# Kernel tuning notes

Hardware: AMD Instinct MI355X
Metric: run time of the kernel (lower is better)

Reference implementation:

```python
import jax, jax.numpy as jnp
import numpy as np

ALPHA = 0.25
GAMMA = 2.0
EPS = 1e-8
W_CLASS = 2.0
W_BBOX = 5.0
W_GIOU = 2.0
PROB_THRESH = 0.5
BBOX_THRESH = -0.1
BIG = 1e9  # cost assigned to filtered-out (masked) pseudo targets


def box_cxcywh_to_xyxy(b):
    cx, cy, w, h = b[..., 0], b[..., 1], b[..., 2], b[..., 3]
    return jnp.stack([cx - 0.5 * w, cy - 0.5 * h, cx + 0.5 * w, cy + 0.5 * h], axis=-1)


def generalized_box_iou(boxes1, boxes2):
    # boxes1: [..., N, 4] xyxy, boxes2: [..., M, 4] xyxy -> [..., N, M]
    area1 = (boxes1[..., 2] - boxes1[..., 0]) * (boxes1[..., 3] - boxes1[..., 1])
    area2 = (boxes2[..., 2] - boxes2[..., 0]) * (boxes2[..., 3] - boxes2[..., 1])
    lt = jnp.maximum(boxes1[..., :, None, :2], boxes2[..., None, :, :2])
    rb = jnp.minimum(boxes1[..., :, None, 2:], boxes2[..., None, :, 2:])
    wh = jnp.clip(rb - lt, 0.0)
    inter = wh[..., 0] * wh[..., 1]
    union = area1[..., :, None] + area2[..., None, :] - inter
    iou = inter / union
    lt_c = jnp.minimum(boxes1[..., :, None, :2], boxes2[..., None, :, :2])
    rb_c = jnp.maximum(boxes1[..., :, None, 2:], boxes2[..., None, :, 2:])
    wh_c = jnp.clip(rb_c - lt_c, 0.0)
    area_c = wh_c[..., 0] * wh_c[..., 1]
    return iou - (area_c - union) / area_c


def setup_inputs() -> dict:
    key = jax.random.key(0)
    k1, k2, k3, k4, k5 = jax.random.split(key, 5)
    B, Q, C, T = 32, 900, 91, 30
    return {
        "pred_logits": jax.random.normal(k1, (B, Q, C), dtype=jnp.float32),
        "pred_boxes": jax.random.uniform(k2, (B, Q, 4), dtype=jnp.float32),
        "pred_logits_base": jax.random.normal(k3, (B, Q, C), dtype=jnp.float32),
        "pred_boxes_base": jax.random.uniform(k4, (B, Q, 4), dtype=jnp.float32),
        "targets_boxes": jax.random.uniform(k5, (B, T, 4), dtype=jnp.float32),
    }


def reference(pred_logits, pred_boxes, pred_logits_base, pred_boxes_base, targets_boxes):
    # ---- pseudo-label generation from the base model (original: sort + python filter) ----
    prob_base = jax.nn.sigmoid(pred_logits_base)          # [B, Qb, C]
    top_prob = jnp.max(prob_base, axis=-1)                # [B, Qb]
    pseudo_labels = jnp.argmax(prob_base, axis=-1)        # [B, Qb] (idx_base[..., 0])
    keep_prob = top_prob > PROB_THRESH
    # original per-box loop: keep if all(-giou(pseudo, gt) > bbox_thresh)
    g_pt = generalized_box_iou(box_cxcywh_to_xyxy(pred_boxes_base),
                               box_cxcywh_to_xyxy(targets_boxes))  # [B, Qb, T]
    keep_giou = jnp.all(-g_pt > BBOX_THRESH, axis=-1)     # [B, Qb]
    pseudo_mask = keep_prob & keep_giou                   # valid pseudo-target slots

    # ---- cost matrix between current predictions and pseudo targets ----
    out_prob = jax.nn.sigmoid(pred_logits)                # [B, Q, C]
    # gather class prob at each pseudo target's label: [B, Q, Qb]
    p = jnp.take_along_axis(out_prob, pseudo_labels[:, None, :], axis=2)
    pos_cost = ALPHA * (1.0 - p) ** GAMMA * (-jnp.log(p + EPS))
    neg_cost = (1.0 - ALPHA) * p ** GAMMA * (-jnp.log(1.0 - p + EPS))
    cost_class = pos_cost - neg_cost

    # L1 cdist between cxcywh boxes: [B, Q, Qb]
    cost_bbox = jnp.sum(jnp.abs(pred_boxes[:, :, None, :] - pred_boxes_base[:, None, :, :]), axis=-1)

    cost_giou = -generalized_box_iou(box_cxcywh_to_xyxy(pred_boxes),
                                     box_cxcywh_to_xyxy(pred_boxes_base))  # [B, Q, Qb]

    C = W_BBOX * cost_bbox + W_CLASS * cost_class + W_GIOU * cost_giou
    # masked (filtered-out) pseudo targets get a huge cost so they are never matched
    C = jnp.where(pseudo_mask[:, None, :], C, BIG)
    return C, pseudo_mask
```

## Files before the change

### kernel.cpp

```cpp
#include <hip/hip_runtime.h>

typedef float f32x4 __attribute__((ext_vector_type(4)));

static constexpr int B  = 32;
static constexpr int Q  = 900;
static constexpr int NC = 91;
static constexpr int T  = 30;
static constexpr int QT = 12;

static constexpr float ALPHA_ = 0.25f;
static constexpr float EPS_   = 1e-8f;
static constexpr float BIG_   = 1e9f;

__global__ __launch_bounds__(256) void k1_mask_label(
    const float* __restrict__ logits_base,
    const float4* __restrict__ boxes_base,
    const float4* __restrict__ targets,
    int* __restrict__ labels,
    float* __restrict__ mask_out) {
#pragma clang fp contract(off)
  int wid  = (blockIdx.x * 256 + threadIdx.x) >> 6;
  int lane = threadIdx.x & 63;
  int b = wid / Q;

  const float* row = logits_base + (size_t)wid * NC;
  float v  = (lane < NC) ? row[lane] : -1e30f;
  int  arg = lane;
  int lane2 = lane + 64;
  if (lane2 < NC) {
    float v2 = row[lane2];
    if (v2 > v) { v = v2; arg = lane2; }
  }
  for (int off = 32; off >= 1; off >>= 1) {
    float ov = __shfl_xor(v, off, 64);
    int   oi = __shfl_xor(arg, off, 64);
    if (ov > v || (ov == v && oi < arg)) { v = ov; arg = oi; }
  }
  bool keep = (v > 0.0f);

  float4 bb = boxes_base[wid];
  float x1 = bb.x - 0.5f * bb.z, y1 = bb.y - 0.5f * bb.w;
  float x2 = bb.x + 0.5f * bb.z, y2 = bb.y + 0.5f * bb.w;
  float a1 = (x2 - x1) * (y2 - y1);

  bool ok = true;
  if (lane < T) {
    float4 tb = targets[b * T + lane];
    float tx1 = tb.x - 0.5f * tb.z, ty1 = tb.y - 0.5f * tb.w;
    float tx2 = tb.x + 0.5f * tb.z, ty2 = tb.y + 0.5f * tb.w;
    float a2 = (tx2 - tx1) * (ty2 - ty1);
    float ltx = fmaxf(x1, tx1), lty = fmaxf(y1, ty1);
    float rbx = fminf(x2, tx2), rby = fminf(y2, ty2);
    float iw = fmaxf(rbx - ltx, 0.0f), ih = fmaxf(rby - lty, 0.0f);
    float inter = iw * ih;
    float uni = (a1 + a2) - inter;
    float iou = inter / uni;
    float cx1 = fminf(x1, tx1), cy1 = fminf(y1, ty1);
    float cx2 = fmaxf(x2, tx2), cy2 = fmaxf(y2, ty2);
    float cw = fmaxf(cx2 - cx1, 0.0f), ch = fmaxf(cy2 - cy1, 0.0f);
    float ac = cw * ch;
    float g = iou - (ac - uni) / ac;
    ok = (-g > -0.1f);
  }
  keep = keep && __all(ok);

  if (lane == 0) {
    labels[wid]   = arg;
    mask_out[wid] = keep ? 1.0f : 0.0f;
  }
}

__device__ __forceinline__ float class_cost(float x) {
  float p   = __builtin_amdgcn_rcpf(1.0f + __expf(-x));
  float omp = 1.0f - p;
  float pos = ALPHA_ * (omp * omp) * (-__logf(p + EPS_));
  float neg = (1.0f - ALPHA_) * (p * p) * (-__logf(omp + EPS_));
  return pos - neg;
}

__global__ __launch_bounds__(256, 4) void k3_cost(
    const float* __restrict__ pred_logits,
    const float4* __restrict__ pred_boxes,
    const float4* __restrict__ boxes_base,
    const int* __restrict__ labels,
    const float* __restrict__ mask_in,
    float* __restrict__ Cout) {
  __shared__ float  s_cc[QT * NC];
  __shared__ float4 s_e[QT];
  __shared__ float4 s_m[QT];
  __shared__ float  s_pa[QT];

  int b   = blockIdx.x / (Q / QT);
  int q0  = (blockIdx.x % (Q / QT)) * QT;
  int tid = threadIdx.x;

  const f32x4* lg4 = reinterpret_cast<const f32x4*>(
      pred_logits + ((size_t)(b * Q + q0)) * NC);
  f32x4* sc4 = reinterpret_cast<f32x4*>(s_cc);
  for (int i = tid; i < QT * NC / 4; i += 256) {
    f32x4 v = __builtin_nontemporal_load(lg4 + i);
    f32x4 o;
    o.x = class_cost(v.x);
    o.y = class_cost(v.y);
    o.z = class_cost(v.z);
    o.w = class_cost(v.w);
    sc4[i] = o;
  }

  if (tid < QT) {
    float4 pb = pred_boxes[b * Q + q0 + tid];
    float px1 = pb.x - 0.5f * pb.z, py1 = pb.y - 0.5f * pb.w;
    float px2 = pb.x + 0.5f * pb.z, py2 = pb.y + 0.5f * pb.w;
    s_e[tid]  = make_float4(px1, py1, px2, py2);
    s_m[tid]  = make_float4(px1 + px2, py1 + py2, pb.z, pb.w);
    s_pa[tid] = (px2 - px1) * (py2 - py1);
  }

  bool active = (tid < Q / 4);
  float x1b[4], y1b[4], x2b[4], y2b[4], wb[4], hb[4], c2big[4];
  const float* pk[4];
  int jbase = b * Q + 4 * tid;
  if (active) {
    int4 lbv = *reinterpret_cast<const int4*>(labels + jbase);
    float4 mkv = *reinterpret_cast<const float4*>(mask_in + jbase);
    pk[0] = s_cc + lbv.x; pk[1] = s_cc + lbv.y;
    pk[2] = s_cc + lbv.z; pk[3] = s_cc + lbv.w;
    c2big[0] = 2.0f + (mkv.x != 0.0f ? 0.0f : BIG_);
    c2big[1] = 2.0f + (mkv.y != 0.0f ? 0.0f : BIG_);
    c2big[2] = 2.0f + (mkv.z != 0.0f ? 0.0f : BIG_);
    c2big[3] = 2.0f + (mkv.w != 0.0f ? 0.0f : BIG_);
#pragma unroll
    for (int k = 0; k < 4; ++k) {
      float4 bb = boxes_base[jbase + k];
      x1b[k] = bb.x - 0.5f * bb.z; y1b[k] = bb.y - 0.5f * bb.w;
      x2b[k] = bb.x + 0.5f * bb.z; y2b[k] = bb.y + 0.5f * bb.w;
      wb[k]  = bb.z; hb[k] = bb.w;
    }
  }
  __syncthreads();

  if (active) {
    size_t rowbase = ((size_t)(b * Q + q0)) * Q + 4 * tid;
#pragma unroll
    for (int qi = 0; qi < QT; ++qi, rowbase += Q) {
      float4 pe = s_e[qi];
      float4 pm = s_m[qi];
      float  pa = s_pa[qi];
      float res[4];
#pragma unroll
      for (int k = 0; k < 4; ++k) {
        float cls = pk[k][qi * NC];
        float dx = pm.x - (x1b[k] + x2b[k]);
        float dy = pm.y - (y1b[k] + y2b[k]);
        float dw = pm.z - wb[k];
        float dh = pm.w - hb[k];
        float l1 = fmaf(0.5f, fabsf(dx) + fabsf(dy), fabsf(dw) + fabsf(dh));
        float mwx = fminf(pe.z, x2b[k]) - fmaxf(pe.x, x1b[k]);
        float mwy = fminf(pe.w, y2b[k]) - fmaxf(pe.y, y1b[k]);
        float inter = fmaxf(mwx, 0.0f) * fmaxf(mwy, 0.0f);
        float uni = fmaf(wb[k], hb[k], pa) - inter;
        float cw = (pm.z + wb[k]) - mwx;
        float ch = (pm.w + hb[k]) - mwy;
        float acl = cw * ch;
        float r = __builtin_amdgcn_rcpf(uni * acl);
        float t = fmaf(inter, acl, uni * uni) * r;
        res[k] = fmaf(-2.0f, t, fmaf(5.0f, l1, fmaf(2.0f, cls, c2big[k])));
      }
      *reinterpret_cast<float4*>(Cout + rowbase) =
          make_float4(res[0], res[1], res[2], res[3]);
    }
  }
}

extern "C" void kernel_launch(void* const* d_in, const int* in_sizes, int n_in,
                              void* d_out, int out_size, void* d_ws, size_t ws_size,
                              hipStream_t stream) {
  const float*  pred_logits      = (const float*)d_in[0];
  const float4* pred_boxes       = (const float4*)d_in[1];
  const float*  pred_logits_base = (const float*)d_in[2];
  const float4* pred_boxes_base  = (const float4*)d_in[3];
  const float4* targets          = (const float4*)d_in[4];

  float* out      = (float*)d_out;
  float* mask_out = out + (size_t)B * Q * Q;

  int* labels = (int*)d_ws;

  k1_mask_label<<<(B * Q) / 4, 256, 0, stream>>>(
      pred_logits_base, pred_boxes_base, targets, labels, mask_out);

  k3_cost<<<B * (Q / QT), 256, 0, stream>>>(
      pred_logits, pred_boxes, pred_boxes_base, labels, mask_out, out);
}
```

Before: 48.24 us.

## Fuse mask/label and cost kernels into one cooperative persistent kernel with grid sync

Merges the pseudo-label/mask kernel and the cost-matrix kernel into a single persistent cooperative launch. Blocks first grid-stride over all pseudo-target rows, then a grid-wide barrier separates that phase from a grid-stride loop over cost tiles. This removes the second kernel launch and the gap between kernels, at the cost of a grid barrier, a fixed grid of up to 4 blocks per CU (assuming 256 CUs), and an extra __syncthreads per tile. The fallback path launches k3_cost twice, which is redundant but only runs if the cooperative launch fails.

```diff
diff --git a/kernel.cpp b/kernel.cpp
--- a/kernel.cpp
+++ b/kernel.cpp
@@ -1,4 +1,7 @@
 #include <hip/hip_runtime.h>
+#include <hip/hip_cooperative_groups.h>
+
+namespace cg = cooperative_groups;
 
 typedef float f32x4 __attribute__((ext_vector_type(4)));
 
@@ -12,15 +15,15 @@
 static constexpr float EPS_   = 1e-8f;
 static constexpr float BIG_   = 1e9f;
 
-__global__ __launch_bounds__(256) void k1_mask_label(
-    const float* __restrict__ logits_base,
-    const float4* __restrict__ boxes_base,
-    const float4* __restrict__ targets,
-    int* __restrict__ labels,
-    float* __restrict__ mask_out) {
+static constexpr int NTILES = B * (Q / QT);
+
+__device__ void mask_label_body(int wid, int lane,
+                                const float* __restrict__ logits_base,
+                                const float4* __restrict__ boxes_base,
+                                const float4* __restrict__ targets,
+                                int* __restrict__ labels,
+                                float* __restrict__ mask_out) {
 #pragma clang fp contract(off)
-  int wid  = (blockIdx.x * 256 + threadIdx.x) >> 6;
-  int lane = threadIdx.x & 63;
   int b = wid / Q;
 
   const float* row = logits_base + (size_t)wid * NC;
@@ -78,21 +81,17 @@
   return pos - neg;
 }
 
-__global__ __launch_bounds__(256, 4) void k3_cost(
-    const float* __restrict__ pred_logits,
-    const float4* __restrict__ pred_boxes,
-    const float4* __restrict__ boxes_base,
-    const int* __restrict__ labels,
-    const float* __restrict__ mask_in,
-    float* __restrict__ Cout) {
-  __shared__ float  s_cc[QT * NC];
-  __shared__ float4 s_e[QT];
-  __shared__ float4 s_m[QT];
-  __shared__ float  s_pa[QT];
-
-  int b   = blockIdx.x / (Q / QT);
-  int q0  = (blockIdx.x % (Q / QT)) * QT;
-  int tid = threadIdx.x;
+__device__ void cost_tile_body(int tile, int tid,
+                               const float* __restrict__ pred_logits,
+                               const float4* __restrict__ pred_boxes,
+                               const float4* __restrict__ boxes_base,
+                               const int* __restrict__ labels,
+                               const float* __restrict__ mask_in,
+                               float* __restrict__ Cout,
+                               float* s_cc, float4* s_e, float4* s_m,
+                               float* s_pa) {
+  int b  = tile / (Q / QT);
+  int q0 = (tile % (Q / QT)) * QT;
 
   const f32x4* lg4 = reinterpret_cast<const f32x4*>(
       pred_logits + ((size_t)(b * Q + q0)) * NC);
@@ -170,6 +169,64 @@
           make_float4(res[0], res[1], res[2], res[3]);
     }
   }
+  __syncthreads();
+}
+
+__global__ __launch_bounds__(256, 4) void fused_all(
+    const float* __restrict__ logits_base,
+    const float4* __restrict__ boxes_base,
+    const float4* __restrict__ targets,
+    int* __restrict__ labels,
+    float* __restrict__ mask_out,
+    const float* __restrict__ pred_logits,
+    const float4* __restrict__ pred_boxes,
+    float* __restrict__ Cout) {
+  __shared__ float  s_cc[QT * NC];
+  __shared__ float4 s_e[QT];
+  __shared__ float4 s_m[QT];
+  __shared__ float  s_pa[QT];
+
+  int tid  = threadIdx.x;
+  int lane = tid & 63;
+
+  int nwaves = gridDim.x * 4;
+  int gw = (blockIdx.x * 256 + tid) >> 6;
+  for (int wid = gw; wid < B * Q; wid += nwaves)
+    mask_label_body(wid, lane, logits_base, boxes_base, targets,
+                    labels, mask_out);
+
+  __threadfence();
+  cg::this_grid().sync();
+
+  for (int tile = blockIdx.x; tile < NTILES; tile += gridDim.x)
+    cost_tile_body(tile, tid, pred_logits, pred_boxes, boxes_base,
+                   labels, mask_out, Cout, s_cc, s_e, s_m, s_pa);
+}
+
+__global__ __launch_bounds__(256) void k1_mask_label(
+    const float* __restrict__ logits_base,
+    const float4* __restrict__ boxes_base,
+    const float4* __restrict__ targets,
+    int* __restrict__ labels,
+    float* __restrict__ mask_out) {
+  int wid  = (blockIdx.x * 256 + threadIdx.x) >> 6;
+  mask_label_body(wid, threadIdx.x & 63, logits_base, boxes_base, targets,
+                  labels, mask_out);
+}
+
+__global__ __launch_bounds__(256, 4) void k3_cost(
+    const float* __restrict__ pred_logits,
+    const float4* __restrict__ pred_boxes,
+    const float4* __restrict__ boxes_base,
+    const int* __restrict__ labels,
+    const float* __restrict__ mask_in,
+    float* __restrict__ Cout) {
+  __shared__ float  s_cc[QT * NC];
+  __shared__ float4 s_e[QT];
+  __shared__ float4 s_m[QT];
+  __shared__ float  s_pa[QT];
+  cost_tile_body(blockIdx.x, threadIdx.x, pred_logits, pred_boxes, boxes_base,
+                 labels, mask_in, Cout, s_cc, s_e, s_m, s_pa);
 }
 
 extern "C" void kernel_launch(void* const* d_in, const int* in_sizes, int n_in,
@@ -186,9 +243,27 @@
 
   int* labels = (int*)d_ws;
 
-  k1_mask_label<<<(B * Q) / 4, 256, 0, stream>>>(
-      pred_logits_base, pred_boxes_base, targets, labels, mask_out);
-
-  k3_cost<<<B * (Q / QT), 256, 0, stream>>>(
-      pred_logits, pred_boxes, pred_boxes_base, labels, mask_out, out);
-}
+  int maxBlk = 0;
+  hipError_t oe = hipOccupancyMaxActiveBlocksPerMultiprocessor(
+      &maxBlk, reinterpret_cast<const void*>(&fused_all), 256, 0);
+  hipError_t le = hipErrorUnknown;
+  if (oe == hipSuccess && maxBlk > 0) {
+    int per_cu = maxBlk < 4 ? maxBlk : 4;
+    int grid   = per_cu * 256;
+    void* args[] = {
+        (void*)&pred_logits_base, (void*)&pred_boxes_base, (void*)&targets,
+        (void*)&labels, (void*)&mask_out,
+        (void*)&pred_logits, (void*)&pred_boxes, (void*)&out};
+    le = hipLaunchCooperativeKernel(reinterpret_cast<const void*>(&fused_all),
+                                    dim3(grid), dim3(256), args, 0, stream);
+  }
+
+  if (le != hipSuccess) {
+    k1_mask_label<<<(B * Q) / 4, 256, 0, stream>>>(
+        pred_logits_base, pred_boxes_base, targets, labels, mask_out);
+    k3_cost<<<NTILES, 256, 0, stream>>>(
+        pred_logits, pred_boxes, pred_boxes_base, labels, mask_out, out);
+    k3_cost<<<NTILES, 256, 0, stream>>>(
+        pred_logits, pred_boxes, pred_boxes_base, labels, mask_out, out);
+  }
+}
```

Measured after the change: 155.9 us. 223% more time.

## Restructure cost kernel so each wave owns four query rows across all targets

Applied to the files above, without the earlier changes.

The cost kernel changes from 12-query-row blocks, where only 225 of 256 threads did work, to a per-wave decomposition. Each wave computes class costs for 4 rows into its own padded shared slice, keeps the pred-box terms in registers, and loops over four 256-column chunks of targets. This fills every lane and launches more, smaller work units. In exchange, the labels, mask and base boxes are reloaded far more often (once per 4 rows instead of once per 12), the last chunk leaves part of the wave idle, and the block-wide syncthreads is no longer needed.

```diff
diff --git a/kernel.cpp b/kernel.cpp
--- a/kernel.cpp
+++ b/kernel.cpp
@@ -6,7 +6,6 @@
 static constexpr int Q  = 900;
 static constexpr int NC = 91;
 static constexpr int T  = 30;
-static constexpr int QT = 12;
 
 static constexpr float ALPHA_ = 0.25f;
 static constexpr float EPS_   = 1e-8f;
@@ -78,96 +77,98 @@
   return pos - neg;
 }
 
-__global__ __launch_bounds__(256, 4) void k3_cost(
+__global__ __launch_bounds__(256) void k3_wave(
     const float* __restrict__ pred_logits,
     const float4* __restrict__ pred_boxes,
     const float4* __restrict__ boxes_base,
     const int* __restrict__ labels,
     const float* __restrict__ mask_in,
     float* __restrict__ Cout) {
-  __shared__ float  s_cc[QT * NC];
-  __shared__ float4 s_e[QT];
-  __shared__ float4 s_m[QT];
-  __shared__ float  s_pa[QT];
+  __shared__ float s_cc[4][4 * 92];
 
-  int b   = blockIdx.x / (Q / QT);
-  int q0  = (blockIdx.x % (Q / QT)) * QT;
-  int tid = threadIdx.x;
+  int tid  = threadIdx.x;
+  int lane = tid & 63;
+  int wv   = tid >> 6;
+  int gwid = blockIdx.x * 4 + wv;
+  int b    = gwid / 225;
+  int row0 = (gwid % 225) * 4;
 
   const f32x4* lg4 = reinterpret_cast<const f32x4*>(
-      pred_logits + ((size_t)(b * Q + q0)) * NC);
-  f32x4* sc4 = reinterpret_cast<f32x4*>(s_cc);
-  for (int i = tid; i < QT * NC / 4; i += 256) {
-    f32x4 v = __builtin_nontemporal_load(lg4 + i);
-    f32x4 o;
-    o.x = class_cost(v.x);
-    o.y = class_cost(v.y);
-    o.z = class_cost(v.z);
-    o.w = class_cost(v.w);
-    sc4[i] = o;
+      pred_logits + ((size_t)(b * Q + row0)) * NC);
+  float* sl = s_cc[wv];
+  for (int i = lane; i < 91; i += 64) {
+    f32x4 v = lg4[i];
+#pragma unroll
+    for (int e = 0; e < 4; ++e) {
+      int f = 4 * i + e;
+      int r = f / 91;
+      int c = f - r * 91;
+      sl[r * 92 + c] = class_cost(v[e]);
+    }
   }
 
-  if (tid < QT) {
-    float4 pb = pred_boxes[b * Q + q0 + tid];
+  float4 pe[4], pm[4];
+  float  pa[4];
+#pragma unroll
+  for (int r = 0; r < 4; ++r) {
+    float4 pb = pred_boxes[b * Q + row0 + r];
     float px1 = pb.x - 0.5f * pb.z, py1 = pb.y - 0.5f * pb.w;
     float px2 = pb.x + 0.5f * pb.z, py2 = pb.y + 0.5f * pb.w;
-    s_e[tid]  = make_float4(px1, py1, px2, py2);
-    s_m[tid]  = make_float4(px1 + px2, py1 + py2, pb.z, pb.w);
-    s_pa[tid] = (px2 - px1) * (py2 - py1);
+    pe[r] = make_float4(px1, py1, px2, py2);
+    pm[r] = make_float4(px1 + px2, py1 + py2, pb.z, pb.w);
+    pa[r] = (px2 - px1) * (py2 - py1);
   }
 
-  bool active = (tid < Q / 4);
-  float x1b[4], y1b[4], x2b[4], y2b[4], wb[4], hb[4], c2big[4];
-  const float* pk[4];
-  int jbase = b * Q + 4 * tid;
-  if (active) {
-    int4 lbv = *reinterpret_cast<const int4*>(labels + jbase);
-    float4 mkv = *reinterpret_cast<const float4*>(mask_in + jbase);
-    pk[0] = s_cc + lbv.x; pk[1] = s_cc + lbv.y;
-    pk[2] = s_cc + lbv.z; pk[3] = s_cc + lbv.w;
-    c2big[0] = 2.0f + (mkv.x != 0.0f ? 0.0f : BIG_);
-    c2big[1] = 2.0f + (mkv.y != 0.0f ? 0.0f : BIG_);
-    c2big[2] = 2.0f + (mkv.z != 0.0f ? 0.0f : BIG_);
-    c2big[3] = 2.0f + (mkv.w != 0.0f ? 0.0f : BIG_);
-#pragma unroll
-    for (int k = 0; k < 4; ++k) {
-      float4 bb = boxes_base[jbase + k];
-      x1b[k] = bb.x - 0.5f * bb.z; y1b[k] = bb.y - 0.5f * bb.w;
-      x2b[k] = bb.x + 0.5f * bb.z; y2b[k] = bb.y + 0.5f * bb.w;
-      wb[k]  = bb.z; hb[k] = bb.w;
-    }
-  }
   __syncthreads();
 
-  if (active) {
-    size_t rowbase = ((size_t)(b * Q + q0)) * Q + 4 * tid;
-#pragma unroll
-    for (int qi = 0; qi < QT; ++qi, rowbase += Q) {
-      float4 pe = s_e[qi];
-      float4 pm = s_m[qi];
-      float  pa = s_pa[qi];
-      float res[4];
+  for (int ch = 0; ch < 4; ++ch) {
+    int qb0 = 256 * ch + 4 * lane;
+    if (qb0 < Q) {
+      int jb = b * Q + qb0;
+      int4   lbv = *reinterpret_cast<const int4*>(labels + jb);
+      float4 mkv = *reinterpret_cast<const float4*>(mask_in + jb);
+      const float* pk[4];
+      pk[0] = sl + lbv.x; pk[1] = sl + lbv.y;
+      pk[2] = sl + lbv.z; pk[3] = sl + lbv.w;
+      float c2big[4];
+      c2big[0] = 2.0f + (mkv.x != 0.0f ? 0.0f : BIG_);
+      c2big[1] = 2.0f + (mkv.y != 0.0f ? 0.0f : BIG_);
+      c2big[2] = 2.0f + (mkv.z != 0.0f ? 0.0f : BIG_);
+      c2big[3] = 2.0f + (mkv.w != 0.0f ? 0.0f : BIG_);
+      float x1b[4], y1b[4], x2b[4], y2b[4], wb[4], hb[4];
 #pragma unroll
       for (int k = 0; k < 4; ++k) {
-        float cls = pk[k][qi * NC];
-        float dx = pm.x - (x1b[k] + x2b[k]);
-        float dy = pm.y - (y1b[k] + y2b[k]);
-        float dw = pm.z - wb[k];
-        float dh = pm.w - hb[k];
-        float l1 = fmaf(0.5f, fabsf(dx) + fabsf(dy), fabsf(dw) + fabsf(dh));
-        float mwx = fminf(pe.z, x2b[k]) - fmaxf(pe.x, x1b[k]);
-        float mwy = fminf(pe.w, y2b[k]) - fmaxf(pe.y, y1b[k]);
-        float inter = fmaxf(mwx, 0.0f) * fmaxf(mwy, 0.0f);
-        float uni = fmaf(wb[k], hb[k], pa) - inter;
-        float cw = (pm.z + wb[k]) - mwx;
-        float ch = (pm.w + hb[k]) - mwy;
-        float acl = cw * ch;
-        float r = __builtin_amdgcn_rcpf(uni * acl);
-        float t = fmaf(inter, acl, uni * uni) * r;
-        res[k] = fmaf(-2.0f, t, fmaf(5.0f, l1, fmaf(2.0f, cls, c2big[k])));
+        float4 bb = boxes_base[jb + k];
+        x1b[k] = bb.x - 0.5f * bb.z; y1b[k] = bb.y - 0.5f * bb.w;
+        x2b[k] = bb.x + 0.5f * bb.z; y2b[k] = bb.y + 0.5f * bb.w;
+        wb[k]  = bb.z; hb[k] = bb.w;
       }
-      *reinterpret_cast<float4*>(Cout + rowbase) =
-          make_float4(res[0], res[1], res[2], res[3]);
+      size_t rowbase = ((size_t)(b * Q + row0)) * Q + qb0;
+#pragma unroll
+      for (int r = 0; r < 4; ++r, rowbase += Q) {
+        float res[4];
+#pragma unroll
+        for (int k = 0; k < 4; ++k) {
+          float cls = pk[k][r * 92];
+          float dx = pm[r].x - (x1b[k] + x2b[k]);
+          float dy = pm[r].y - (y1b[k] + y2b[k]);
+          float dw = pm[r].z - wb[k];
+          float dh = pm[r].w - hb[k];
+          float l1 = fmaf(0.5f, fabsf(dx) + fabsf(dy), fabsf(dw) + fabsf(dh));
+          float mwx = fminf(pe[r].z, x2b[k]) - fmaxf(pe[r].x, x1b[k]);
+          float mwy = fminf(pe[r].w, y2b[k]) - fmaxf(pe[r].y, y1b[k]);
+          float inter = fmaxf(mwx, 0.0f) * fmaxf(mwy, 0.0f);
+          float uni = fmaf(wb[k], hb[k], pa[r]) - inter;
+          float cw = (pm[r].z + wb[k]) - mwx;
+          float chh = (pm[r].w + hb[k]) - mwy;
+          float acl = cw * chh;
+          float rr = __builtin_amdgcn_rcpf(uni * acl);
+          float t = fmaf(inter, acl, uni * uni) * rr;
+          res[k] = fmaf(-2.0f, t, fmaf(5.0f, l1, fmaf(2.0f, cls, c2big[k])));
+        }
+        *reinterpret_cast<float4*>(Cout + rowbase) =
+            make_float4(res[0], res[1], res[2], res[3]);
+      }
     }
   }
 }
@@ -189,6 +190,6 @@
   k1_mask_label<<<(B * Q) / 4, 256, 0, stream>>>(
       pred_logits_base, pred_boxes_base, targets, labels, mask_out);
 
-  k3_cost<<<B * (Q / QT), 256, 0, stream>>>(
+  k3_wave<<<1800, 256, 0, stream>>>(
       pred_logits, pred_boxes, pred_boxes_base, labels, mask_out, out);
 }
```

New measurement: 50.26 us. 4.2% more time.
